# Kernel optimization log

Measured on AMD Instinct MI355X. Metric: run time of the kernel, lower is better.

Reference implementation:

```python
import jax, jax.numpy as jnp
import numpy as np

S, E, H, D, L = 2048, 1024, 16, 64, 6  # seq, embed(=H*D), heads, d_model, stack
FF = 4 * E
EPS = 1e-5


def _pos_embedding():
    pos = jnp.arange(S, dtype=jnp.float32)[:, None]
    idx = jnp.arange(E, dtype=jnp.float32)[None, :]
    ang = pos / jnp.power(10000.0, idx / E)
    # even positions -> sin row, odd positions -> cos row (as in the source)
    return jnp.where(jnp.arange(S)[:, None] % 2 == 0, jnp.sin(ang), jnp.cos(ang))


def _layer_norm(x, g, b):
    mu = jnp.mean(x, axis=-1, keepdims=True)
    var = jnp.mean(jnp.square(x - mu), axis=-1, keepdims=True)
    return (x - mu) * jax.lax.rsqrt(var + EPS) * g + b


def setup_inputs() -> dict:
    key = jax.random.key(0)
    ks = jax.random.split(key, 12)
    n = lambda k, shape, s=0.02: jax.random.normal(k, shape, jnp.float32) * s
    return {
        "x": jax.random.normal(ks[0], (S, E), jnp.float32),
        # shared (default-arg trap) input projections [d_model, embed]
        "Wk": n(ks[1], (D, E)), "Wq": n(ks[2], (D, E)), "Wv": n(ks[3], (D, E)),
        # per-layer per-head linears (stored [in,out])
        "hWk": n(ks[4], (L, H, D, D)), "hbk": jnp.zeros((L, H, D), jnp.float32),
        "hWq": n(ks[5], (L, H, D, D)), "hbq": jnp.zeros((L, H, D), jnp.float32),
        "hWv": n(ks[6], (L, H, D, D)), "hbv": jnp.zeros((L, H, D), jnp.float32),
        "Wo": n(ks[7], (L, E, E)), "bo": jnp.zeros((L, E), jnp.float32),
        "ln1_g": jnp.ones((L, E), jnp.float32), "ln1_b": jnp.zeros((L, E), jnp.float32),
        "W1": n(ks[8], (L, E, FF)), "b1": jnp.zeros((L, FF), jnp.float32),
        "W2": n(ks[9], (L, FF, E)), "b2": jnp.zeros((L, E), jnp.float32),
        "ln2_g": jnp.ones((L, E), jnp.float32), "ln2_b": jnp.zeros((L, E), jnp.float32),
    }


def reference(x, Wk, Wq, Wv, hWk, hbk, hWq, hbq, hWv, hbv, Wo, bo,
              ln1_g, ln1_b, W1, b1, W2, b2, ln2_g, ln2_b):
    h = x + _pos_embedding()
    scale = 1.0 / jnp.sqrt(jnp.float32(D))
    for l in range(L):
        # shared projections: [S, D]
        K = h @ Wk.T
        Q = h @ Wq.T
        V = h @ Wv.T
        # per-head linears: [H, S, D]
        kh = jnp.einsum('sd,hde->hse', K, hWk[l]) + hbk[l][:, None, :]
        qh = jnp.einsum('sd,hde->hse', Q, hWq[l]) + hbq[l][:, None, :]
        vh = jnp.einsum('sd,hde->hse', V, hWv[l]) + hbv[l][:, None, :]
        scores = jnp.einsum('hqd,hkd->hqk', qh, kh) * scale  # [H, S, S]
        attn = jax.nn.softmax(scores, axis=-1)
        out = jnp.einsum('hqk,hkd->hqd', attn, vh)           # [H, S, D]
        cat = jnp.transpose(out, (1, 0, 2)).reshape(S, H * D)  # [S, E]
        o = cat @ Wo[l] + bo[l]
        h = _layer_norm(o + h, ln1_g[l], ln1_b[l])
        # FFN
        f = jax.nn.relu(h @ W1[l] + b1[l]) @ W2[l] + b2[l]
        h = _layer_norm(f + h, ln2_g[l], ln2_b[l])
    return h
```

## Files before the change

kernel.cpp:

```cpp
#include <hip/hip_runtime.h>
#include <stdint.h>

typedef unsigned short u16;
typedef unsigned int   u32;

constexpr int SS = 2048, EE = 1024, HH = 16, DD = 64, LL = 6, FF = 4096;

typedef __bf16 bf16x8 __attribute__((ext_vector_type(8)));
typedef float  f32x4  __attribute__((ext_vector_type(4)));

#define DEV __device__ __forceinline__
#define AS1 __attribute__((address_space(1)))
#define AS3 __attribute__((address_space(3)))

DEV u16 f2bf(float f) {
    u32 u = __builtin_bit_cast(u32, f);
    u += 0x7FFFu + ((u >> 16) & 1u);
    return (u16)(u >> 16);
}

DEV float bf2f(u16 v) { return __builtin_bit_cast(float, (u32)v << 16); }

DEV void store_bf4(u16* p, float a, float b, float c, float d) {
    u32 lo = (u32)f2bf(a) | ((u32)f2bf(b) << 16);
    u32 hi = (u32)f2bf(c) | ((u32)f2bf(d) << 16);
    *(uint2*)p = make_uint2(lo, hi);
}

DEV void gload16(const void* g, void* l) {
    __builtin_amdgcn_global_load_lds((const AS1 void*)g, (AS3 void*)l, 16, 0, 0);
}

DEV f32x4 mfma16(bf16x8 a, bf16x8 b, f32x4 c) {
    return __builtin_amdgcn_mfma_f32_16x16x32_bf16(a, b, c, 0, 0, 0);
}

DEV float exp2_fast(float x) {
    float r;
    asm("v_exp_f32 %0, %1" : "=v"(r) : "v"(x));
    return r;
}

DEV int kvperm(int c) {
    return (c & 32) | ((c & 12) << 1) | ((c & 16) >> 2) | (c & 3);
}

DEV int xcd_swz(int flat, int nwg) {
    int chunk = nwg >> 3;
    return (flat & 7) * chunk + (flat >> 3);
}

constexpr size_t ALGN(size_t x) { return (x + 255) & ~(size_t)255; }
constexpr size_t OFF_WF   = 0;
constexpr size_t OFF_HWT  = ALGN(OFF_WF   + (size_t)3*LL*1024*1024*2);
constexpr size_t OFF_WSHT = ALGN(OFF_HWT  + (size_t)3*96*4096*2);
constexpr size_t OFF_HB   = ALGN(OFF_WSHT + (size_t)3*1024*64*2);
constexpr size_t OFF_WOT  = ALGN(OFF_HB   + (size_t)LL*3*HH*64*4);
constexpr size_t OFF_W1T  = ALGN(OFF_WOT  + (size_t)LL*EE*EE*2);
constexpr size_t OFF_W2T  = ALGN(OFF_W1T  + (size_t)LL*FF*EE*2);
constexpr size_t OFF_HBF  = ALGN(OFF_W2T  + (size_t)LL*EE*FF*2);
constexpr size_t OFF_QKVH = ALGN(OFF_HBF  + (size_t)SS*EE*2);
constexpr size_t OFF_VT   = OFF_QKVH + (size_t)2*HH*SS*64*2;
constexpr size_t OFF_CAT  = OFF_VT   + (size_t)1024*SS*2;
constexpr size_t OFF_F1   = OFF_QKVH;
constexpr size_t OFF_OF   = ALGN(OFF_CAT + (size_t)SS*EE*2);

__global__ void pos_add(const float* __restrict__ x, u16* __restrict__ hb) {
    const int row = blockIdx.x, tid = threadIdx.x;
    float4 x4 = ((const float4*)(x + (size_t)row * EE))[tid];
    float v[4] = {x4.x, x4.y, x4.z, x4.w};
    float y[4];
#pragma unroll
    for (int j = 0; j < 4; ++j) {
        int e = tid * 4 + j;
        float ang = (float)row * expf((float)e * (-9.210340371976184f / 1024.f));
        float pe = ((row & 1) == 0) ? sinf(ang) : cosf(ang);
        y[j] = v[j] + pe;
    }
    store_bf4(hb + (size_t)row * EE + tid * 4, y[0], y[1], y[2], y[3]);
}

__global__ void pack_bias(const float* __restrict__ bk, const float* __restrict__ bq,
                          const float* __restrict__ bv, float* __restrict__ dst) {
    int i = blockIdx.x * 256 + threadIdx.x;
    if (i >= LL * 3 * HH * 64) return;
    int d = i & 63;
    int hh = (i >> 6) & 15;
    int lt = i >> 10;
    int t = lt % 3, l = lt / 3;
    const float* s = (t == 0) ? bk : (t == 1) ? bq : bv;
    dst[i] = s[((size_t)l * HH + hh) * 64 + d];
}

DEV void tile_t64(const float* src, u16* dst, int R, int C, int c0, int r0,
                  float (*t)[65], int tid) {
    const int lr = tid >> 4, lc4 = (tid & 15) * 4;
#pragma unroll
    for (int i = 0; i < 4; ++i) {
        int r = i * 16 + lr;
        float4 v = *(const float4*)(src + (size_t)(r0 + r) * C + c0 + lc4);
        t[r][lc4] = v.x; t[r][lc4 + 1] = v.y; t[r][lc4 + 2] = v.z; t[r][lc4 + 3] = v.w;
    }
    __syncthreads();
    const int cr = tid >> 3, rr8 = (tid & 7) * 8;
#pragma unroll
    for (int i = 0; i < 2; ++i) {
        int cc = i * 32 + cr;
        u16 tmp[8];
#pragma unroll
        for (int j = 0; j < 8; ++j) tmp[j] = f2bf(t[rr8 + j][cc]);
        *(uint4*)(dst + (size_t)(c0 + cc) * R + r0 + rr8) = *(uint4*)tmp;
    }
}

__global__ void transpose_cast64(const float* __restrict__ src, u16* __restrict__ dst,
                                 int R, int C, long sSrc, long sDst) {
    __shared__ float t[64][65];
    const int b = blockIdx.z;
    tile_t64(src + (size_t)b * sSrc, dst + (size_t)b * sDst, R, C,
             blockIdx.x * 64, blockIdx.y * 64, t, threadIdx.x);
}

__global__ void hw_t3(const float* __restrict__ s0, const float* __restrict__ s1,
                      const float* __restrict__ s2, u16* __restrict__ dst) {
    __shared__ float t[64][65];
    const int z = blockIdx.z;
    const float* src = (z < 96 ? s0 : z < 192 ? s1 : s2) + (size_t)(z % 96) * 4096;
    tile_t64(src, dst + (size_t)z * 4096, 64, 64, 0, 0, t, threadIdx.x);
}

__global__ void wsh_t3(const float* __restrict__ s0, const float* __restrict__ s1,
                       const float* __restrict__ s2, u16* __restrict__ dst) {
    __shared__ float t[64][65];
    const int z = blockIdx.z;
    const float* src = (z == 0) ? s0 : (z == 1) ? s1 : s2;
    tile_t64(src, dst + (size_t)z * 65536, 64, 1024, blockIdx.x * 64, 0, t, threadIdx.x);
}

template<int BIASMODE, bool RELU, bool SPLITK, bool BATCH>
__launch_bounds__(256)
__global__ void gemm_std(const u16* __restrict__ A, const u16* __restrict__ B,
                         const float* __restrict__ bias, u16* __restrict__ Cb,
                         int M, int N, int K, int lda, int ldb,
                         long zsA, long zsB, long zsC) {
    __shared__ u16 As[2][128 * 64];
    __shared__ u16 Bs[2][128 * 64];
    const int gx = gridDim.x;
    const int swz = xcd_swz(blockIdx.y * gx + blockIdx.x, gx * gridDim.y);
    const int bn = swz % gx, bm = swz / gx, z = blockIdx.z;
    const int tid = threadIdx.x, w = tid >> 6;
    const int lane = tid & 63, l15 = lane & 15, hi = lane >> 4;
    const int wm = w >> 1, wn = w & 1;
    const u16* Ab = A + (size_t)bm * 128 * lda + (SPLITK ? (size_t)z * K : 0) + (BATCH ? (size_t)z * zsA : 0);
    const u16* Bb = B + (size_t)bn * 128 * ldb + (SPLITK ? (size_t)z * K : 0) + (BATCH ? (size_t)z * zsB : 0);
    const size_t coff = SPLITK ? (size_t)z * M * N : (BATCH ? (size_t)z * zsC : 0);
    const int tr = tid >> 3, tp = tid & 7;

    f32x4 acc[4][4];
#pragma unroll
    for (int i = 0; i < 4; ++i)
#pragma unroll
        for (int j = 0; j < 4; ++j) acc[i][j] = f32x4{0.f, 0.f, 0.f, 0.f};

    auto STAGE = [&](int b, int kt) {
        const u16* Abk = Ab + kt + (size_t)tr * lda + tp * 8;
        const u16* Bbk = Bb + kt + (size_t)tr * ldb + tp * 8;
#pragma unroll
        for (int i = 0; i < 4; ++i) {
            gload16(Abk + (size_t)i * 32 * lda, &As[b][(i * 256 + w * 64) * 8]);
            gload16(Bbk + (size_t)i * 32 * ldb, &Bs[b][(i * 256 + w * 64) * 8]);
        }
    };

    STAGE(0, 0);
    __syncthreads();
    int buf = 0;

    for (int kt = 0; kt < K; kt += 64) {
        if (kt + 64 < K) STAGE(buf ^ 1, kt + 64);
#pragma unroll
        for (int kk = 0; kk < 2; ++kk) {
            bf16x8 af[4], bf[4];
#pragma unroll
            for (int mi = 0; mi < 4; ++mi)
                af[mi] = *(const bf16x8*)&As[buf][(wm * 64 + mi * 16 + l15) * 64 + kk * 32 + hi * 8];
#pragma unroll
            for (int ni = 0; ni < 4; ++ni)
                bf[ni] = *(const bf16x8*)&Bs[buf][(wn * 64 + ni * 16 + l15) * 64 + kk * 32 + hi * 8];
#pragma unroll
            for (int mi = 0; mi < 4; ++mi)
#pragma unroll
                for (int ni = 0; ni < 4; ++ni)
                    acc[mi][ni] = mfma16(af[mi], bf[ni], acc[mi][ni]);
        }
        __syncthreads();
        buf ^= 1;
    }

#pragma unroll
    for (int mi = 0; mi < 4; ++mi) {
        int rg = bm * 128 + wm * 64 + mi * 16 + hi * 4;
#pragma unroll
        for (int ni = 0; ni < 4; ++ni) {
            int cg = bn * 128 + wn * 64 + ni * 16 + l15;
            float bc = (BIASMODE == 1) ? bias[cg] : 0.f;
#pragma unroll
            for (int r = 0; r < 4; ++r) {
                float v = acc[mi][ni][r] + bc;
                if (RELU) v = fmaxf(v, 0.f);
                Cb[coff + (size_t)(rg + r) * N + cg] = f2bf(v);
            }
        }
    }
}

__launch_bounds__(256)
__global__ void gemm_qkv(const u16* __restrict__ A, const u16* __restrict__ WF, int l,
                         const float* __restrict__ bias, u16* __restrict__ QKVH,
                         u16* __restrict__ VT) {
    __shared__ u16 As[2][128 * 64];
    __shared__ u16 Bs[2][128 * 64];
    const int gx = gridDim.x;
    const int swz = xcd_swz(blockIdx.y * gx + blockIdx.x, gx * gridDim.y);
    const int bn = swz % gx, bm = swz / gx;
    const int tid = threadIdx.x, w = tid >> 6;
    const int lane = tid & 63, l15 = lane & 15, hi = lane >> 4;
    const int wm = w >> 1, wn = w & 1;
    const int t = bn >> 3;
    const u16* Ab = A + (size_t)bm * 128 * 1024;
    const u16* Bb = WF + (((size_t)(t * 6 + l)) << 20) + (size_t)(bn & 7) * 128 * 1024;
    const int tr = tid >> 3, tp = tid & 7;

    f32x4 acc[4][4];
#pragma unroll
    for (int i = 0; i < 4; ++i)
#pragma unroll
        for (int j = 0; j < 4; ++j) acc[i][j] = f32x4{0.f, 0.f, 0.f, 0.f};

    auto STAGE = [&](int b, int kt) {
        const u16* Abk = Ab + kt + (size_t)tr * 1024 + tp * 8;
        const u16* Bbk = Bb + kt + (size_t)tr * 1024 + tp * 8;
#pragma unroll
        for (int i = 0; i < 4; ++i) {
            gload16(Abk + (size_t)i * 32 * 1024, &As[b][(i * 256 + w * 64) * 8]);
            gload16(Bbk + (size_t)i * 32 * 1024, &Bs[b][(i * 256 + w * 64) * 8]);
        }
    };

    STAGE(0, 0);
    __syncthreads();
    int buf = 0;

    for (int kt = 0; kt < 1024; kt += 64) {
        if (kt + 64 < 1024) STAGE(buf ^ 1, kt + 64);
#pragma unroll
        for (int kk = 0; kk < 2; ++kk) {
            bf16x8 af[4], bf[4];
#pragma unroll
            for (int mi = 0; mi < 4; ++mi)
                af[mi] = *(const bf16x8*)&As[buf][(wm * 64 + mi * 16 + l15) * 64 + kk * 32 + hi * 8];
#pragma unroll
            for (int ni = 0; ni < 4; ++ni)
                bf[ni] = *(const bf16x8*)&Bs[buf][(wn * 64 + ni * 16 + l15) * 64 + kk * 32 + hi * 8];
#pragma unroll
            for (int mi = 0; mi < 4; ++mi)
#pragma unroll
                for (int ni = 0; ni < 4; ++ni)
                    acc[mi][ni] = mfma16(af[mi], bf[ni], acc[mi][ni]);
        }
        __syncthreads();
        buf ^= 1;
    }

    if (t < 2) {
        const float sc = (t == 1) ? 0.18033688011112042f : 1.f;
#pragma unroll
        for (int mi = 0; mi < 4; ++mi) {
            int rg = bm * 128 + wm * 64 + mi * 16 + hi * 4;
#pragma unroll
            for (int ni = 0; ni < 4; ++ni) {
                int cg = bn * 128 + wn * 64 + ni * 16 + l15;
                int hd = cg & 1023, hh = hd >> 6, d = hd & 63;
                float bv = bias[cg];
                u16* dst = QKVH + (((size_t)(t * 16 + hh) * SS) + rg) * 64 + d;
#pragma unroll
                for (int r = 0; r < 4; ++r)
                    dst[(size_t)r * 64] = f2bf((acc[mi][ni][r] + bv) * sc);
            }
        }
    } else {
#pragma unroll
        for (int mi = 0; mi < 4; ++mi) {
            int s0 = bm * 128 + wm * 64 + mi * 16 + hi * 4;
            int ps = (s0 & ~63) | kvperm(s0 & 63);
#pragma unroll
            for (int ni = 0; ni < 4; ++ni) {
                int cg = bn * 128 + wn * 64 + ni * 16 + l15;
                int hd = cg & 1023;
                float bv = bias[cg];
                u16 tmp[4];
#pragma unroll
                for (int r = 0; r < 4; ++r) tmp[r] = f2bf(acc[mi][ni][r] + bv);
                *(uint2*)(VT + (size_t)hd * SS + ps) = *(uint2*)tmp;
            }
        }
    }
}

__launch_bounds__(256)
__global__ void attn_fwd(const u16* __restrict__ QKVH, const u16* __restrict__ VT,
                         u16* __restrict__ cat) {
    const int logical = (blockIdx.x & 7) * 64 + (blockIdx.x >> 3);
    const int h = logical >> 5, qt = logical & 31;
    const int tid = threadIdx.x, w = tid >> 6, lane = tid & 63;
    const int l15 = lane & 15, hi = lane >> 4;
    __shared__ __align__(16) u16 smem[33824];

    const u16* qb = QKVH + (((size_t)(16 + h) * SS) + qt * 64) * 64;
    const u16* kb = QKVH + ((size_t)h * SS) * 64;
    const u16* vb = VT + (size_t)h * 64 * SS;

    bf16x8 bq[4][2];
#pragma unroll
    for (int qg = 0; qg < 4; ++qg) {
        bq[qg][0] = *(const bf16x8*)(qb + (qg * 16 + l15) * 64 + hi * 8);
        bq[qg][1] = *(const bf16x8*)(qb + (qg * 16 + l15) * 64 + 32 + hi * 8);
    }
    bf16x8 ONES;
#pragma unroll
    for (int i = 0; i < 8; ++i) ONES[i] = (__bf16)1.0f;

    f32x4 oacc[4][4];
#pragma unroll
    for (int i = 0; i < 4; ++i)
#pragma unroll
        for (int j = 0; j < 4; ++j) oacc[i][j] = f32x4{0.f, 0.f, 0.f, 0.f};
    f32x4 sacc[4];
#pragma unroll
    for (int i = 0; i < 4; ++i) sacc[i] = f32x4{0.f, 0.f, 0.f, 0.f};
    float mrun = 0.f;

    auto STAGE = [&](int buf, int t) {
#pragma unroll
        for (int j = 0; j < 4; ++j) {
            int fl = j * 256 + tid;
            int kr = fl >> 3, kc = (fl & 7) ^ (kr & 7);
            gload16(kb + ((size_t)(t * 128 + kr)) * 64 + kc * 8, smem + buf * 8192 + fl * 8);
            int vr = fl >> 4, vc = (fl & 15) ^ (vr & 7);
            gload16(vb + (size_t)vr * SS + t * 128 + vc * 8, smem + 16384 + buf * 8192 + fl * 8);
        }
    };

    STAGE(0, 0);
    __syncthreads();
    int buf = 0;
    const int kbase = w * 32;

    for (int t = 0; t < SS / 128; ++t) {
        if (t < SS / 128 - 1) STAGE(buf ^ 1, t + 1);
        const u16* ks = smem + buf * 8192;
        const u16* vs = smem + 16384 + buf * 8192;

        bf16x8 kf[2][2];
#pragma unroll
        for (int kvg = 0; kvg < 2; ++kvg) {
            int row = kbase + kvg * 16 + l15;
            const u16* kr = ks + row * 64;
            kf[kvg][0] = *(const bf16x8*)&kr[((0 * 4 + hi) ^ (row & 7)) * 8];
            kf[kvg][1] = *(const bf16x8*)&kr[((1 * 4 + hi) ^ (row & 7)) * 8];
        }

        f32x4 sc[4][2];
        __builtin_amdgcn_s_setprio(1);
#pragma unroll
        for (int qg = 0; qg < 4; ++qg)
#pragma unroll
            for (int kvg = 0; kvg < 2; ++kvg) {
                f32x4 a = f32x4{0.f, 0.f, 0.f, 0.f};
                a = mfma16(kf[kvg][0], bq[qg][0], a);
                a = mfma16(kf[kvg][1], bq[qg][1], a);
                sc[qg][kvg] = a;
            }
        __builtin_amdgcn_s_setprio(0);

        bf16x8 pa[4];
#pragma unroll
        for (int qg = 0; qg < 4; ++qg) {
            bf16x8 v;
#pragma unroll
            for (int r = 0; r < 4; ++r) {
                v[r]     = (__bf16)exp2_fast(sc[qg][0][r] - mrun);
                v[4 + r] = (__bf16)exp2_fast(sc[qg][1][r] - mrun);
            }
            pa[qg] = v;
        }

        bf16x8 bv[4];
#pragma unroll
        for (int di = 0; di < 4; ++di) {
            int d = di * 16 + l15;
            bv[di] = *(const bf16x8*)&vs[d * 128 + (((w * 4 + hi) ^ (d & 7)) * 8)];
        }

        __builtin_amdgcn_s_setprio(1);
#pragma unroll
        for (int qg = 0; qg < 4; ++qg) {
            sacc[qg] = mfma16(pa[qg], ONES, sacc[qg]);
#pragma unroll
            for (int di = 0; di < 4; ++di)
                oacc[qg][di] = mfma16(pa[qg], bv[di], oacc[qg][di]);
        }
        __builtin_amdgcn_s_setprio(0);

        float mx = sacc[0][0];
#pragma unroll
        for (int qg = 0; qg < 4; ++qg)
#pragma unroll
            for (int r = 0; r < 4; ++r) mx = fmaxf(mx, sacc[qg][r]);
        if (__any(mx > 1.0e30f)) {
            const float dn = 5.421010862427522e-20f;
            mrun += 64.f;
#pragma unroll
            for (int qg = 0; qg < 4; ++qg) {
#pragma unroll
                for (int r = 0; r < 4; ++r) sacc[qg][r] *= dn;
#pragma unroll
                for (int di = 0; di < 4; ++di)
#pragma unroll
                    for (int r = 0; r < 4; ++r) oacc[qg][di][r] *= dn;
            }
        }

        __syncthreads();
        buf ^= 1;
    }

    float* P4   = (float*)smem;
    float* sred = P4 + 4 * 64 * 65;
    float* smr  = sred + 4 * 64;
#pragma unroll
    for (int qg = 0; qg < 4; ++qg) {
        int q = qg * 16 + hi * 4;
#pragma unroll
        for (int di = 0; di < 4; ++di)
#pragma unroll
            for (int r = 0; r < 4; ++r)
                P4[(size_t)(w * 64 + q + r) * 65 + di * 16 + l15] = oacc[qg][di][r];
        if (l15 == 0) {
#pragma unroll
            for (int r = 0; r < 4; ++r) sred[w * 64 + q + r] = sacc[qg][r];
        }
    }
    if (lane == 0) smr[w] = mrun;
    __syncthreads();

    float mmax = fmaxf(fmaxf(smr[0], smr[1]), fmaxf(smr[2], smr[3]));
    float wsc[4];
#pragma unroll
    for (int sw = 0; sw < 4; ++sw) wsc[sw] = exp2_fast(smr[sw] - mmax);

    float rs[4];
#pragma unroll
    for (int r = 0; r < 4; ++r) {
        int q = w * 16 + hi * 4 + r;
        float s = 0.f;
#pragma unroll
        for (int sw = 0; sw < 4; ++sw) s += sred[sw * 64 + q] * wsc[sw];
        rs[r] = 1.f / s;
    }
#pragma unroll
    for (int di = 0; di < 4; ++di) {
        int col = h * 64 + di * 16 + l15;
#pragma unroll
        for (int r = 0; r < 4; ++r) {
            int q = w * 16 + hi * 4 + r;
            float o = 0.f;
#pragma unroll
            for (int sw = 0; sw < 4; ++sw)
                o += P4[(size_t)(sw * 64 + q) * 65 + di * 16 + l15] * wsc[sw];
            cat[(size_t)(qt * 64 + q) * EE + col] = f2bf(o * rs[r]);
        }
    }
}

template<bool FINAL>
__launch_bounds__(256)
__global__ void add_ln4(const u16* __restrict__ o, const float* __restrict__ ob,
                        const u16* __restrict__ res,
                        const float* __restrict__ g, const float* __restrict__ b,
                        float* __restrict__ fout, u16* __restrict__ hb) {
    const int row = blockIdx.x, tid = threadIdx.x;
    const int w = tid >> 6, lane = tid & 63;
    float x0, x1, x2, x3;
    {
        ushort4 r4 = ((const ushort4*)(res + (size_t)row * EE))[tid];
        float4 ob4 = ((const float4*)ob)[tid];
        x0 = bf2f(r4.x) + ob4.x; x1 = bf2f(r4.y) + ob4.y;
        x2 = bf2f(r4.z) + ob4.z; x3 = bf2f(r4.w) + ob4.w;
    }
#pragma unroll
    for (int z = 0; z < 4; ++z) {
        ushort4 a4 = ((const ushort4*)(o + (size_t)z * SS * EE + (size_t)row * EE))[tid];
        x0 += bf2f(a4.x); x1 += bf2f(a4.y); x2 += bf2f(a4.z); x3 += bf2f(a4.w);
    }
    float s = x0 + x1 + x2 + x3;
    float q = x0 * x0 + x1 * x1 + x2 * x2 + x3 * x3;
#pragma unroll
    for (int off = 1; off < 64; off <<= 1) { s += __shfl_xor(s, off); q += __shfl_xor(q, off); }
    __shared__ float red[8];
    if (lane == 0) { red[w] = s; red[4 + w] = q; }
    __syncthreads();
    s = red[0] + red[1] + red[2] + red[3];
    q = red[4] + red[5] + red[6] + red[7];
    const float mu = s * (1.f / EE);
    const float var = q * (1.f / EE) - mu * mu;
    const float rstd = rsqrtf(var + 1e-5f);
    const int c0 = tid * 4;
    float y0 = (x0 - mu) * rstd * g[c0 + 0] + b[c0 + 0];
    float y1 = (x1 - mu) * rstd * g[c0 + 1] + b[c0 + 1];
    float y2 = (x2 - mu) * rstd * g[c0 + 2] + b[c0 + 2];
    float y3 = (x3 - mu) * rstd * g[c0 + 3] + b[c0 + 3];
    if (FINAL) ((float4*)(fout + (size_t)row * EE))[tid] = make_float4(y0, y1, y2, y3);
    store_bf4(hb + (size_t)row * EE + c0, y0, y1, y2, y3);
}

extern "C" void kernel_launch(void* const* d_in, const int* in_sizes, int n_in,
                              void* d_out, int out_size, void* d_ws, size_t ws_size,
                              hipStream_t stream) {
    const float* x    = (const float*)d_in[0];
    const float* Wk   = (const float*)d_in[1];
    const float* Wq   = (const float*)d_in[2];
    const float* Wv   = (const float*)d_in[3];
    const float* hWk  = (const float*)d_in[4];
    const float* hbk  = (const float*)d_in[5];
    const float* hWq  = (const float*)d_in[6];
    const float* hbq  = (const float*)d_in[7];
    const float* hWv  = (const float*)d_in[8];
    const float* hbv  = (const float*)d_in[9];
    const float* Wo   = (const float*)d_in[10];
    const float* bo   = (const float*)d_in[11];
    const float* ln1g = (const float*)d_in[12];
    const float* ln1b = (const float*)d_in[13];
    const float* W1   = (const float*)d_in[14];
    const float* b1   = (const float*)d_in[15];
    const float* W2   = (const float*)d_in[16];
    const float* b2   = (const float*)d_in[17];
    const float* ln2g = (const float*)d_in[18];
    const float* ln2b = (const float*)d_in[19];

    char* ws = (char*)d_ws;
    u16*   WF   = (u16*)(ws + OFF_WF);
    u16*   HWT  = (u16*)(ws + OFF_HWT);
    u16*   WSHT = (u16*)(ws + OFF_WSHT);
    float* HB   = (float*)(ws + OFF_HB);
    u16*   WOT  = (u16*)(ws + OFF_WOT);
    u16*   W1T  = (u16*)(ws + OFF_W1T);
    u16*   W2T  = (u16*)(ws + OFF_W2T);
    u16*   HBF  = (u16*)(ws + OFF_HBF);
    u16*   QKVH = (u16*)(ws + OFF_QKVH);
    u16*   VT   = (u16*)(ws + OFF_VT);
    u16*   CAT  = (u16*)(ws + OFF_CAT);
    u16*   F1   = (u16*)(ws + OFF_F1);
    u16*   OFb  = (u16*)(ws + OFF_OF);

    pos_add<<<SS, 256, 0, stream>>>(x, HBF);
    pack_bias<<<72, 256, 0, stream>>>(hbk, hbq, hbv, HB);
    hw_t3<<<dim3(1, 1, 288), 256, 0, stream>>>(hWk, hWq, hWv, HWT);
    wsh_t3<<<dim3(16, 1, 3), 256, 0, stream>>>(Wk, Wq, Wv, WSHT);
    gemm_std<0, false, false, true><<<dim3(8, 48, 3), 256, 0, stream>>>(
        HWT, WSHT, nullptr, WF, 6144, 1024, 64, 64, 64,
        (long)96 * 4096, 65536, (long)6144 * 1024);
    transpose_cast64<<<dim3(16, 16, LL), 256, 0, stream>>>(Wo, WOT, EE, EE, (long)EE * EE, (long)EE * EE);
    transpose_cast64<<<dim3(64, 16, LL), 256, 0, stream>>>(W1, W1T, EE, FF, (long)EE * FF, (long)FF * EE);
    transpose_cast64<<<dim3(16, 64, LL), 256, 0, stream>>>(W2, W2T, FF, EE, (long)FF * EE, (long)EE * FF);

    for (int l = 0; l < LL; ++l) {
        gemm_qkv<<<dim3(24, 16, 1), 256, 0, stream>>>(HBF, WF, l, HB + (size_t)l * 3072, QKVH, VT);

        attn_fwd<<<512, 256, 0, stream>>>(QKVH, VT, CAT);

        gemm_std<0, false, true, false><<<dim3(8, 16, 4), 256, 0, stream>>>(
            CAT, WOT + (size_t)l * EE * EE, nullptr, OFb, SS, EE, 256, 1024, 1024, 0, 0, 0);
        add_ln4<false><<<SS, 256, 0, stream>>>(OFb, bo + (size_t)l * EE, HBF,
                                               ln1g + (size_t)l * EE, ln1b + (size_t)l * EE,
                                               nullptr, HBF);

        gemm_std<1, true, false, false><<<dim3(32, 16, 1), 256, 0, stream>>>(
            HBF, W1T + (size_t)l * FF * EE, b1 + (size_t)l * FF, F1, SS, FF, 1024, 1024, 1024, 0, 0, 0);
        gemm_std<0, false, true, false><<<dim3(8, 16, 4), 256, 0, stream>>>(
            F1, W2T + (size_t)l * EE * FF, nullptr, OFb, SS, EE, 1024, 4096, 4096, 0, 0, 0);
        if (l == LL - 1)
            add_ln4<true><<<SS, 256, 0, stream>>>(OFb, b2 + (size_t)l * EE, HBF,
                                                  ln2g + (size_t)l * EE, ln2b + (size_t)l * EE,
                                                  (float*)d_out, HBF);
        else
            add_ln4<false><<<SS, 256, 0, stream>>>(OFb, b2 + (size_t)l * EE, HBF,
                                                   ln2g + (size_t)l * EE, ln2b + (size_t)l * EE,
                                                   nullptr, HBF);
    }
}
```

Measured before the change: 930.8 us.

## Fold per-head V weights into Wo and split QKV projection into small GEMMs

Since softmax rows sum to one, the per-head V linear (and its bias) is folded into the output projection: Wo is premultiplied by hWv per head and the V bias is folded into bo. As a result V is computed once as a shared [S,64] tensor instead of per head. The fused QKV GEMM over precomposed weights is replaced by a two-stage path: a shared K/Q/V projection to 64 columns, then a small batched per-head GEMM for K and Q. This cuts the per-layer projection FLOPs at the cost of extra launches, small-tile GEMM efficiency, and extra one-time prep work.

Result: no change. 917.3 us (-1.4%).

```diff
diff --git a/kernel.cpp b/kernel.cpp
--- a/kernel.cpp
+++ b/kernel.cpp
@@ -51,19 +51,22 @@
 }
 
 constexpr size_t ALGN(size_t x) { return (x + 255) & ~(size_t)255; }
-constexpr size_t OFF_WF   = 0;
-constexpr size_t OFF_HWT  = ALGN(OFF_WF   + (size_t)3*LL*1024*1024*2);
-constexpr size_t OFF_WSHT = ALGN(OFF_HWT  + (size_t)3*96*4096*2);
-constexpr size_t OFF_HB   = ALGN(OFF_WSHT + (size_t)3*1024*64*2);
+constexpr size_t OFF_WSHB = 0;
+constexpr size_t OFF_HVB  = ALGN(OFF_WSHB + (size_t)3*64*1024*2);
+constexpr size_t OFF_KQV3 = ALGN(OFF_HVB  + (size_t)96*4096*2);
+constexpr size_t OFF_WVOT = ALGN(OFF_KQV3 + (size_t)3*SS*64*2);
+constexpr size_t OFF_BO2  = ALGN(OFF_WVOT + (size_t)LL*EE*EE*2);
+constexpr size_t OFF_HWT  = ALGN(OFF_BO2  + (size_t)LL*EE*4);
+constexpr size_t OFF_HB   = ALGN(OFF_HWT  + (size_t)3*96*4096*2);
 constexpr size_t OFF_WOT  = ALGN(OFF_HB   + (size_t)LL*3*HH*64*4);
 constexpr size_t OFF_W1T  = ALGN(OFF_WOT  + (size_t)LL*EE*EE*2);
 constexpr size_t OFF_W2T  = ALGN(OFF_W1T  + (size_t)LL*FF*EE*2);
 constexpr size_t OFF_HBF  = ALGN(OFF_W2T  + (size_t)LL*EE*FF*2);
 constexpr size_t OFF_QKVH = ALGN(OFF_HBF  + (size_t)SS*EE*2);
 constexpr size_t OFF_VT   = OFF_QKVH + (size_t)2*HH*SS*64*2;
-constexpr size_t OFF_CAT  = OFF_VT   + (size_t)1024*SS*2;
+constexpr size_t OFF_CAT  = OFF_VT   + (size_t)64*SS*2;
 constexpr size_t OFF_F1   = OFF_QKVH;
-constexpr size_t OFF_OF   = ALGN(OFF_CAT + (size_t)SS*EE*2);
+constexpr size_t OFF_OF   = ALGN(OFF_F1  + (size_t)SS*FF*2);
 
 __global__ void pos_add(const float* __restrict__ x, u16* __restrict__ hb) {
     const int row = blockIdx.x, tid = threadIdx.x;
@@ -129,12 +132,28 @@
     tile_t64(src, dst + (size_t)z * 4096, 64, 64, 0, 0, t, threadIdx.x);
 }
 
-__global__ void wsh_t3(const float* __restrict__ s0, const float* __restrict__ s1,
-                       const float* __restrict__ s2, u16* __restrict__ dst) {
-    __shared__ float t[64][65];
-    const int z = blockIdx.z;
-    const float* src = (z == 0) ? s0 : (z == 1) ? s1 : s2;
-    tile_t64(src, dst + (size_t)z * 65536, 64, 1024, blockIdx.x * 64, 0, t, threadIdx.x);
+__global__ void wsh_cast(const float* __restrict__ s0, const float* __restrict__ s1,
+                         const float* __restrict__ s2, u16* __restrict__ dst) {
+    const int z = blockIdx.z, row = blockIdx.x, tid = threadIdx.x;
+    const float* s = (z == 0 ? s0 : z == 1 ? s1 : s2) + (size_t)row * 1024 + tid * 4;
+    float4 v = *(const float4*)s;
+    store_bf4(dst + ((size_t)z * 64 + row) * 1024 + tid * 4, v.x, v.y, v.z, v.w);
+}
+
+__global__ void hv_cast(const float* __restrict__ src, u16* __restrict__ dst) {
+    size_t i = ((size_t)blockIdx.x * 256 + threadIdx.x) * 4;
+    float4 v = *(const float4*)(src + i);
+    store_bf4(dst + i, v.x, v.y, v.z, v.w);
+}
+
+__global__ void bo_fold(const float* __restrict__ bo, const float* __restrict__ hbv,
+                        const float* __restrict__ Wo, float* __restrict__ BO2) {
+    const int l = blockIdx.z, e = blockIdx.x * 256 + threadIdx.x;
+    float acc = bo[(size_t)l * EE + e];
+    const float* w = Wo + (size_t)l * EE * EE + e;
+    const float* bv = hbv + (size_t)l * EE;
+    for (int j = 0; j < EE; ++j) acc += bv[j] * w[(size_t)j * EE];
+    BO2[(size_t)l * EE + e] = acc;
 }
 
 template<int BIASMODE, bool RELU, bool SPLITK, bool BATCH>
@@ -214,36 +233,37 @@
     }
 }
 
+template<int EPI>
 __launch_bounds__(256)
-__global__ void gemm_qkv(const u16* __restrict__ A, const u16* __restrict__ WF, int l,
-                         const float* __restrict__ bias, u16* __restrict__ QKVH,
-                         u16* __restrict__ VT) {
-    __shared__ u16 As[2][128 * 64];
-    __shared__ u16 Bs[2][128 * 64];
-    const int gx = gridDim.x;
-    const int swz = xcd_swz(blockIdx.y * gx + blockIdx.x, gx * gridDim.y);
-    const int bn = swz % gx, bm = swz / gx;
+__global__ void gemm_small(const u16* __restrict__ A, const u16* __restrict__ B,
+                           const float* __restrict__ bias, u16* __restrict__ C0,
+                           u16* __restrict__ C1,
+                           int K, int lda, int ldb, int ldc, int zdiv,
+                           long aL, long aS, long bL, long bS, long cL, long cS) {
+    __shared__ u16 As[2][64 * 64];
+    __shared__ u16 Bs[2][64 * 64];
+    const int bm = blockIdx.x, z = blockIdx.z;
+    const int zq = z / zdiv, zr = z % zdiv;
     const int tid = threadIdx.x, w = tid >> 6;
     const int lane = tid & 63, l15 = lane & 15, hi = lane >> 4;
     const int wm = w >> 1, wn = w & 1;
-    const int t = bn >> 3;
-    const u16* Ab = A + (size_t)bm * 128 * 1024;
-    const u16* Bb = WF + (((size_t)(t * 6 + l)) << 20) + (size_t)(bn & 7) * 128 * 1024;
+    const u16* Ab = A + (size_t)bm * 64 * lda + (size_t)zq * aL + (size_t)zr * aS;
+    const u16* Bb = B + (size_t)zq * bL + (size_t)zr * bS;
     const int tr = tid >> 3, tp = tid & 7;
 
-    f32x4 acc[4][4];
-#pragma unroll
-    for (int i = 0; i < 4; ++i)
-#pragma unroll
-        for (int j = 0; j < 4; ++j) acc[i][j] = f32x4{0.f, 0.f, 0.f, 0.f};
+    f32x4 acc[2][2];
+#pragma unroll
+    for (int i = 0; i < 2; ++i)
+#pragma unroll
+        for (int j = 0; j < 2; ++j) acc[i][j] = f32x4{0.f, 0.f, 0.f, 0.f};
 
     auto STAGE = [&](int b, int kt) {
-        const u16* Abk = Ab + kt + (size_t)tr * 1024 + tp * 8;
-        const u16* Bbk = Bb + kt + (size_t)tr * 1024 + tp * 8;
-#pragma unroll
-        for (int i = 0; i < 4; ++i) {
-            gload16(Abk + (size_t)i * 32 * 1024, &As[b][(i * 256 + w * 64) * 8]);
-            gload16(Bbk + (size_t)i * 32 * 1024, &Bs[b][(i * 256 + w * 64) * 8]);
+        const u16* Abk = Ab + kt + (size_t)tr * lda + tp * 8;
+        const u16* Bbk = Bb + kt + (size_t)tr * ldb + tp * 8;
+#pragma unroll
+        for (int i = 0; i < 2; ++i) {
+            gload16(Abk + (size_t)i * 32 * lda, &As[b][(i * 256 + tid) * 8]);
+            gload16(Bbk + (size_t)i * 32 * ldb, &Bs[b][(i * 256 + tid) * 8]);
         }
     };
 
@@ -251,57 +271,57 @@
     __syncthreads();
     int buf = 0;
 
-    for (int kt = 0; kt < 1024; kt += 64) {
-        if (kt + 64 < 1024) STAGE(buf ^ 1, kt + 64);
+    for (int kt = 0; kt < K; kt += 64) {
+        if (kt + 64 < K) STAGE(buf ^ 1, kt + 64);
 #pragma unroll
         for (int kk = 0; kk < 2; ++kk) {
-            bf16x8 af[4], bf[4];
-#pragma unroll
-            for (int mi = 0; mi < 4; ++mi)
-                af[mi] = *(const bf16x8*)&As[buf][(wm * 64 + mi * 16 + l15) * 64 + kk * 32 + hi * 8];
-#pragma unroll
-            for (int ni = 0; ni < 4; ++ni)
-                bf[ni] = *(const bf16x8*)&Bs[buf][(wn * 64 + ni * 16 + l15) * 64 + kk * 32 + hi * 8];
-#pragma unroll
-            for (int mi = 0; mi < 4; ++mi)
-#pragma unroll
-                for (int ni = 0; ni < 4; ++ni)
+            bf16x8 af[2], bf[2];
+#pragma unroll
+            for (int mi = 0; mi < 2; ++mi)
+                af[mi] = *(const bf16x8*)&As[buf][(wm * 32 + mi * 16 + l15) * 64 + kk * 32 + hi * 8];
+#pragma unroll
+            for (int ni = 0; ni < 2; ++ni)
+                bf[ni] = *(const bf16x8*)&Bs[buf][(wn * 32 + ni * 16 + l15) * 64 + kk * 32 + hi * 8];
+#pragma unroll
+            for (int mi = 0; mi < 2; ++mi)
+#pragma unroll
+                for (int ni = 0; ni < 2; ++ni)
                     acc[mi][ni] = mfma16(af[mi], bf[ni], acc[mi][ni]);
         }
         __syncthreads();
         buf ^= 1;
     }
 
-    if (t < 2) {
-        const float sc = (t == 1) ? 0.18033688011112042f : 1.f;
-#pragma unroll
-        for (int mi = 0; mi < 4; ++mi) {
-            int rg = bm * 128 + wm * 64 + mi * 16 + hi * 4;
-#pragma unroll
-            for (int ni = 0; ni < 4; ++ni) {
-                int cg = bn * 128 + wn * 64 + ni * 16 + l15;
-                int hd = cg & 1023, hh = hd >> 6, d = hd & 63;
-                float bv = bias[cg];
-                u16* dst = QKVH + (((size_t)(t * 16 + hh) * SS) + rg) * 64 + d;
+#pragma unroll
+    for (int mi = 0; mi < 2; ++mi) {
+        const int rg = bm * 64 + wm * 32 + mi * 16 + hi * 4;
+#pragma unroll
+        for (int ni = 0; ni < 2; ++ni) {
+            const int cn = wn * 32 + ni * 16 + l15;
+            if (EPI == 0) {
+#pragma unroll
+                for (int r = 0; r < 4; ++r)
+                    C0[(size_t)zq * cL + (size_t)zr * cS + (size_t)(rg + r) * ldc + cn] =
+                        f2bf(acc[mi][ni][r]);
+            } else if (EPI == 1) {
+                const float sc = (z >= 16) ? 0.18033688011112042f : 1.f;
+                const float bv = bias[z * 64 + cn];
+                u16* dst = C0 + ((size_t)z * SS + rg) * 64 + cn;
 #pragma unroll
                 for (int r = 0; r < 4; ++r)
                     dst[(size_t)r * 64] = f2bf((acc[mi][ni][r] + bv) * sc);
-            }
-        }
-    } else {
-#pragma unroll
-        for (int mi = 0; mi < 4; ++mi) {
-            int s0 = bm * 128 + wm * 64 + mi * 16 + hi * 4;
-            int ps = (s0 & ~63) | kvperm(s0 & 63);
-#pragma unroll
-            for (int ni = 0; ni < 4; ++ni) {
-                int cg = bn * 128 + wn * 64 + ni * 16 + l15;
-                int hd = cg & 1023;
-                float bv = bias[cg];
-                u16 tmp[4];
-#pragma unroll
-                for (int r = 0; r < 4; ++r) tmp[r] = f2bf(acc[mi][ni][r] + bv);
-                *(uint2*)(VT + (size_t)hd * SS + ps) = *(uint2*)tmp;
+            } else {
+                if (z < 2) {
+#pragma unroll
+                    for (int r = 0; r < 4; ++r)
+                        C0[(size_t)z * SS * 64 + (size_t)(rg + r) * 64 + cn] = f2bf(acc[mi][ni][r]);
+                } else {
+                    const int ps = (rg & ~63) | kvperm(rg & 63);
+                    u16 tmp[4];
+#pragma unroll
+                    for (int r = 0; r < 4; ++r) tmp[r] = f2bf(acc[mi][ni][r]);
+                    *(uint2*)(C1 + (size_t)cn * SS + ps) = *(uint2*)tmp;
+                }
             }
         }
     }
@@ -318,7 +338,7 @@
 
     const u16* qb = QKVH + (((size_t)(16 + h) * SS) + qt * 64) * 64;
     const u16* kb = QKVH + ((size_t)h * SS) * 64;
-    const u16* vb = VT + (size_t)h * 64 * SS;
+    const u16* vb = VT;
 
     bf16x8 bq[4][2];
 #pragma unroll
@@ -549,9 +569,12 @@
     const float* ln2b = (const float*)d_in[19];
 
     char* ws = (char*)d_ws;
-    u16*   WF   = (u16*)(ws + OFF_WF);
+    u16*   WSHB = (u16*)(ws + OFF_WSHB);
+    u16*   HVB  = (u16*)(ws + OFF_HVB);
+    u16*   KQV3 = (u16*)(ws + OFF_KQV3);
+    u16*   WVOT = (u16*)(ws + OFF_WVOT);
+    float* BO2  = (float*)(ws + OFF_BO2);
     u16*   HWT  = (u16*)(ws + OFF_HWT);
-    u16*   WSHT = (u16*)(ws + OFF_WSHT);
     float* HB   = (float*)(ws + OFF_HB);
     u16*   WOT  = (u16*)(ws + OFF_WOT);
     u16*   W1T  = (u16*)(ws + OFF_W1T);
@@ -565,23 +588,31 @@
 
     pos_add<<<SS, 256, 0, stream>>>(x, HBF);
     pack_bias<<<72, 256, 0, stream>>>(hbk, hbq, hbv, HB);
-    hw_t3<<<dim3(1, 1, 288), 256, 0, stream>>>(hWk, hWq, hWv, HWT);
-    wsh_t3<<<dim3(16, 1, 3), 256, 0, stream>>>(Wk, Wq, Wv, WSHT);
-    gemm_std<0, false, false, true><<<dim3(8, 48, 3), 256, 0, stream>>>(
-        HWT, WSHT, nullptr, WF, 6144, 1024, 64, 64, 64,
-        (long)96 * 4096, 65536, (long)6144 * 1024);
+    hw_t3<<<dim3(1, 1, 192), 256, 0, stream>>>(hWk, hWq, hWv, HWT);
+    wsh_cast<<<dim3(64, 1, 3), 256, 0, stream>>>(Wk, Wq, Wv, WSHB);
+    hv_cast<<<384, 256, 0, stream>>>(hWv, HVB);
+    bo_fold<<<dim3(4, 1, LL), 256, 0, stream>>>(bo, hbv, Wo, BO2);
     transpose_cast64<<<dim3(16, 16, LL), 256, 0, stream>>>(Wo, WOT, EE, EE, (long)EE * EE, (long)EE * EE);
     transpose_cast64<<<dim3(64, 16, LL), 256, 0, stream>>>(W1, W1T, EE, FF, (long)EE * FF, (long)FF * EE);
     transpose_cast64<<<dim3(16, 64, LL), 256, 0, stream>>>(W2, W2T, FF, EE, (long)FF * EE, (long)EE * FF);
+    gemm_small<0><<<dim3(16, 1, 96), 256, 0, stream>>>(
+        WOT, HVB, nullptr, WVOT, nullptr, 64, 1024, 64, 1024, 16,
+        (long)EE * EE, 64, (long)16 * 4096, 4096, (long)EE * EE, 64);
 
     for (int l = 0; l < LL; ++l) {
-        gemm_qkv<<<dim3(24, 16, 1), 256, 0, stream>>>(HBF, WF, l, HB + (size_t)l * 3072, QKVH, VT);
+        gemm_small<3><<<dim3(32, 1, 3), 256, 0, stream>>>(
+            HBF, WSHB, nullptr, KQV3, VT, 1024, 1024, 1024, 64, 64,
+            0, 0, 0, (long)64 * 1024, 0, 0);
+        gemm_small<1><<<dim3(32, 1, 32), 256, 0, stream>>>(
+            KQV3, HWT + (size_t)l * 16 * 4096, HB + (size_t)l * 3072, QKVH, nullptr,
+            64, 64, 64, 64, 16,
+            (long)SS * 64, 0, (long)96 * 4096, 4096, 0, 0);
 
         attn_fwd<<<512, 256, 0, stream>>>(QKVH, VT, CAT);
 
         gemm_std<0, false, true, false><<<dim3(8, 16, 4), 256, 0, stream>>>(
-            CAT, WOT + (size_t)l * EE * EE, nullptr, OFb, SS, EE, 256, 1024, 1024, 0, 0, 0);
-        add_ln4<false><<<SS, 256, 0, stream>>>(OFb, bo + (size_t)l * EE, HBF,
+            CAT, WVOT + (size_t)l * EE * EE, nullptr, OFb, SS, EE, 256, 1024, 1024, 0, 0, 0);
+        add_ln4<false><<<SS, 256, 0, stream>>>(OFb, BO2 + (size_t)l * EE, HBF,
                                                ln1g + (size_t)l * EE, ln1b + (size_t)l * EE,
                                                nullptr, HBF);
 
```
